# Performance work log

Hardware: AMD Instinct MI355X
Metric: run time of the kernel (lower is better)

Reference implementation:

```python
import jax, jax.numpy as jnp
import numpy as np

B, T, D, H = 8, 1024, 1024, 16
DH = D // H
EPS = 1e-5


def setup_inputs() -> dict:
    key = jax.random.key(0)
    ks = jax.random.split(key, 8)
    s = 0.02
    return {
        "x": jax.random.normal(ks[0], (B, T, D), dtype=jnp.float32),
        # per-head Q/K/V weights stacked: (H, in_c, d_head), applied as x @ W
        "Wq": jax.random.normal(ks[1], (H, D, DH), dtype=jnp.float32) * s,
        "Wk": jax.random.normal(ks[2], (H, D, DH), dtype=jnp.float32) * s,
        "Wv": jax.random.normal(ks[3], (H, D, DH), dtype=jnp.float32) * s,
        # FFN weights stored (in, out): y = x @ W
        "W1": jax.random.normal(ks[4], (D, D), dtype=jnp.float32) * s,
        "W2": jax.random.normal(ks[5], (D, D), dtype=jnp.float32) * s,
        "g1": jnp.ones((D,), jnp.float32),
        "b1": jnp.zeros((D,), jnp.float32),
        "g2": jnp.ones((D,), jnp.float32),
        "b2": jnp.zeros((D,), jnp.float32),
    }


def _layer_norm(x, g, b):
    m = jnp.mean(x, axis=-1, keepdims=True)
    v = jnp.mean((x - m) ** 2, axis=-1, keepdims=True)  # biased, as torch LN
    return (x - m) * jax.lax.rsqrt(v + EPS) * g + b


def reference(x, Wq, Wk, Wv, W1, W2, g1, b1, g2, b2):
    b, t, d = x.shape
    dh = Wq.shape[-1]
    q = jnp.einsum("btc,hcd->bhtd", x, Wq)
    k = jnp.einsum("btc,hcd->bhtd", x, Wk)
    v = jnp.einsum("btc,hcd->bhtd", x, Wv)
    attn = jnp.einsum("bhtd,bhsd->bhts", q, k) / (dh ** 0.5)
    # Original: attn @ ones(T,T) -> every column equals rowsum(attn);
    # softmax(dim=1) over the query axis is then constant across columns,
    # so out[t] = softmax_t(rowsum)[t] * sum_s v[s]. Same math, reduced.
    rowsum = attn.sum(axis=-1)               # (B,H,T)
    p = jax.nn.softmax(rowsum, axis=-1)      # softmax over query index t
    vsum = v.sum(axis=2)                     # (B,H,DH)
    head_out = p[..., None] * vsum[:, :, None, :]        # (B,H,T,DH)
    out = head_out.transpose(0, 2, 1, 3).reshape(b, t, d)  # concat heads
    x1 = _layer_norm(x + out, g1, b1)
    ff = jax.nn.relu(x1 @ W1) @ W2           # dropout = identity (eval)
    return _layer_norm(x1 + ff, g2, b2)
```

## Files before the change

### kernel.cpp

```cpp
#include <hip/hip_runtime.h>

#define NB 8
#define NT 1024
#define ND 1024
#define NH 16
#define NDH 64
#define NM (NB*NT)
#define LNEPS 1e-5f

typedef __attribute__((ext_vector_type(8))) __bf16 bf16x8;
typedef __attribute__((ext_vector_type(4))) float f32x4;

__global__ void transpose_to_bf16(const float* __restrict__ W1, const float* __restrict__ W2,
                                  __bf16* __restrict__ WT1, __bf16* __restrict__ WT2) {
    __shared__ float tile[32][33];
    const float* W = blockIdx.z ? W2 : W1;
    __bf16* WT = blockIdx.z ? WT2 : WT1;
    int bx = blockIdx.x * 32;
    int by = blockIdx.y * 32;
    int tx = threadIdx.x;
    int ty = threadIdx.y;
    for (int i = ty; i < 32; i += 8)
        tile[i][tx] = W[(size_t)(by + i) * ND + bx + tx];
    __syncthreads();
    for (int i = ty; i < 32; i += 8)
        WT[(size_t)(bx + i) * ND + by + tx] = (__bf16)tile[tx][i];
}

__global__ void xsum_kernel(const float* __restrict__ x, float* __restrict__ xsum) {
    int b = blockIdx.x;
    int chunk = blockIdx.y;
    int tid = threadIdx.x;
    const float4* xp = (const float4*)(x + ((size_t)b * NT + chunk * 16) * ND) + tid;
    float4 s = {0.f, 0.f, 0.f, 0.f};
    #pragma unroll
    for (int t = 0; t < 16; ++t) {
        float4 v = xp[(size_t)t * (ND / 4)];
        s.x += v.x; s.y += v.y; s.z += v.z; s.w += v.w;
    }
    float* dst = xsum + b * ND + tid * 4;
    atomicAdd(dst + 0, s.x);
    atomicAdd(dst + 1, s.y);
    atomicAdd(dst + 2, s.z);
    atomicAdd(dst + 3, s.w);
}

__global__ __launch_bounds__(256) void ksum_vsum_kernel(const float* __restrict__ xsum,
                                                        const float* __restrict__ Wk,
                                                        const float* __restrict__ Wv,
                                                        float* __restrict__ ksumg,
                                                        float* __restrict__ vsumg) {
    int h = blockIdx.x, cs = blockIdx.y;
    int t = threadIdx.x, lane = t & 63, w = t >> 6;
    int c0 = cs * 64;
    __shared__ float xs[8][64];
    #pragma unroll
    for (int i = 0; i < 2; ++i) {
        int idx = t + i * 256;
        xs[idx >> 6][idx & 63] = xsum[(idx >> 6) * ND + c0 + (idx & 63)];
    }
    __syncthreads();
    float sk[8] = {}, sv[8] = {};
    #pragma unroll 4
    for (int j = 0; j < 16; ++j) {
        int c = c0 + w * 16 + j;
        float wk = Wk[((size_t)h * ND + c) * NDH + lane];
        float wv = Wv[((size_t)h * ND + c) * NDH + lane];
        #pragma unroll
        for (int b = 0; b < 8; ++b) {
            float xv = xs[b][w * 16 + j];
            sk[b] += xv * wk;
            sv[b] += xv * wv;
        }
    }
    __shared__ float red[2][8][4][64];
    #pragma unroll
    for (int b = 0; b < 8; ++b) {
        red[0][b][w][lane] = sk[b];
        red[1][b][w][lane] = sv[b];
    }
    __syncthreads();
    #pragma unroll
    for (int i = 0; i < 4; ++i) {
        int o = t + i * 256;
        int d = o & 63, rest = o >> 6;
        int a = rest >> 3, b = rest & 7;
        float s = red[a][b][0][d] + red[a][b][1][d] + red[a][b][2][d] + red[a][b][3][d];
        float* dst = a ? vsumg : ksumg;
        atomicAdd(&dst[((size_t)b * NH + h) * NDH + d], s);
    }
}

__global__ __launch_bounds__(256) void wqk_kernel(const float* __restrict__ ksumg,
                                                  const float* __restrict__ Wq,
                                                  float* __restrict__ wqk) {
    int h = blockIdx.x, b = blockIdx.y, cs = blockIdx.z;
    int t = threadIdx.x;
    __shared__ float ks[NDH];
    if (t < 64) ks[t] = ksumg[((size_t)b * NH + h) * NDH + t];
    __syncthreads();
    #pragma unroll
    for (int i = 0; i < 2; ++i) {
        int c = cs * 512 + i * 256 + t;
        const float4* wq = (const float4*)(Wq + ((size_t)h * ND + c) * NDH);
        float s = 0.f;
        #pragma unroll
        for (int dq = 0; dq < 16; ++dq) {
            float4 v = wq[dq];
            s += v.x * ks[dq * 4] + v.y * ks[dq * 4 + 1] +
                 v.z * ks[dq * 4 + 2] + v.w * ks[dq * 4 + 3];
        }
        wqk[((size_t)b * NH + h) * ND + c] = s * 0.125f;
    }
}

__global__ __launch_bounds__(256) void rowsum_kernel(const float* __restrict__ x,
                                                     const float* __restrict__ wqk,
                                                     float* __restrict__ rowsum) {
    int tc = blockIdx.x, b = blockIdx.y;
    int tid = threadIdx.x, wid = tid >> 6, lane = tid & 63;
    int t0 = tc * 16 + wid * 4;
    float acc[4][16];
    #pragma unroll
    for (int tq = 0; tq < 4; ++tq)
        #pragma unroll
        for (int h = 0; h < 16; ++h) acc[tq][h] = 0.f;
    const float4* wb = (const float4*)(wqk + (size_t)b * NH * ND);
    #pragma unroll
    for (int chunk = 0; chunk < 4; ++chunk) {
        float4 xv[4];
        #pragma unroll
        for (int tq = 0; tq < 4; ++tq)
            xv[tq] = ((const float4*)(x + ((size_t)b * NT + t0 + tq) * ND))[chunk * 64 + lane];
        #pragma unroll
        for (int h = 0; h < 16; ++h) {
            float4 wv = wb[h * 256 + chunk * 64 + lane];
            #pragma unroll
            for (int tq = 0; tq < 4; ++tq)
                acc[tq][h] += xv[tq].x * wv.x + xv[tq].y * wv.y +
                              xv[tq].z * wv.z + xv[tq].w * wv.w;
        }
    }
    bool c0 = lane & 1, c1 = lane & 2, c2 = lane & 4, c3 = lane & 8;
    float out4[4];
    #pragma unroll
    for (int tq = 0; tq < 4; ++tq) {
        float w8[8];
        #pragma unroll
        for (int j = 0; j < 8; ++j) {
            float send = c0 ? acc[tq][2 * j] : acc[tq][2 * j + 1];
            float recv = __shfl_xor(send, 1, 64);
            w8[j] = (c0 ? acc[tq][2 * j + 1] : acc[tq][2 * j]) + recv;
        }
        float u4[4];
        #pragma unroll
        for (int j = 0; j < 4; ++j) {
            float send = c1 ? w8[2 * j] : w8[2 * j + 1];
            float recv = __shfl_xor(send, 2, 64);
            u4[j] = (c1 ? w8[2 * j + 1] : w8[2 * j]) + recv;
        }
        float s2[2];
        #pragma unroll
        for (int j = 0; j < 2; ++j) {
            float send = c2 ? u4[2 * j] : u4[2 * j + 1];
            float recv = __shfl_xor(send, 4, 64);
            s2[j] = (c2 ? u4[2 * j + 1] : u4[2 * j]) + recv;
        }
        float send = c3 ? s2[0] : s2[1];
        float recv = __shfl_xor(send, 8, 64);
        float r = (c3 ? s2[1] : s2[0]) + recv;
        r += __shfl_xor(r, 16, 64);
        r += __shfl_xor(r, 32, 64);
        out4[tq] = r;
    }
    if (lane < 16) {
        float4 o = {out4[0], out4[1], out4[2], out4[3]};
        *(float4*)(rowsum + ((size_t)b * NH + lane) * NT + t0) = o;
    }
}

__global__ void softmax_kernel(float* __restrict__ rs) {
    int bh = blockIdx.x, tid = threadIdx.x;
    int wave = tid >> 6, lane = tid & 63;
    float* row = rs + (size_t)bh * NT;
    float4 v = ((float4*)row)[tid];
    float m = fmaxf(fmaxf(v.x, v.y), fmaxf(v.z, v.w));
    __shared__ float red[4];
    for (int off = 32; off; off >>= 1) m = fmaxf(m, __shfl_down(m, off, 64));
    if (lane == 0) red[wave] = m;
    __syncthreads();
    m = fmaxf(fmaxf(red[0], red[1]), fmaxf(red[2], red[3]));
    __syncthreads();
    float4 e;
    e.x = __expf(v.x - m); e.y = __expf(v.y - m);
    e.z = __expf(v.z - m); e.w = __expf(v.w - m);
    float s = e.x + e.y + e.z + e.w;
    for (int off = 32; off; off >>= 1) s += __shfl_down(s, off, 64);
    if (lane == 0) red[wave] = s;
    __syncthreads();
    s = red[0] + red[1] + red[2] + red[3];
    float inv = 1.f / s;
    e.x *= inv; e.y *= inv; e.z *= inv; e.w *= inv;
    ((float4*)row)[tid] = e;
}

__global__ void ln1_kernel(const float* __restrict__ x, const float* __restrict__ p,
                           const float* __restrict__ vsum,
                           const float* __restrict__ g1, const float* __restrict__ b1,
                           __bf16* __restrict__ x1b) {
    int t = blockIdx.x, b = blockIdx.y, tid = threadIdx.x;
    int wave = tid >> 6, lane = tid & 63;
    size_t rowoff = ((size_t)b * NT + t) * ND;
    float4 xv = ((const float4*)(x + rowoff))[tid];
    int h = tid >> 4;
    float pv = p[((size_t)b * NH + h) * NT + t];
    float4 vs = ((const float4*)(vsum + ((size_t)b * NH + h) * NDH))[tid & 15];
    float4 s;
    s.x = xv.x + pv * vs.x; s.y = xv.y + pv * vs.y;
    s.z = xv.z + pv * vs.z; s.w = xv.w + pv * vs.w;
    float sum = s.x + s.y + s.z + s.w;
    float sq = s.x * s.x + s.y * s.y + s.z * s.z + s.w * s.w;
    __shared__ float rs_[4], rq_[4];
    for (int off = 32; off; off >>= 1) {
        sum += __shfl_down(sum, off, 64);
        sq += __shfl_down(sq, off, 64);
    }
    if (lane == 0) { rs_[wave] = sum; rq_[wave] = sq; }
    __syncthreads();
    sum = rs_[0] + rs_[1] + rs_[2] + rs_[3];
    sq = rq_[0] + rq_[1] + rq_[2] + rq_[3];
    float mu = sum * (1.f / ND);
    float var = sq * (1.f / ND) - mu * mu;
    float rstd = rsqrtf(var + LNEPS);
    float4 g = ((const float4*)g1)[tid];
    float4 bb = ((const float4*)b1)[tid];
    union { __bf16 h4[4]; uint2 u; } pk;
    pk.h4[0] = (__bf16)((s.x - mu) * rstd * g.x + bb.x);
    pk.h4[1] = (__bf16)((s.y - mu) * rstd * g.y + bb.y);
    pk.h4[2] = (__bf16)((s.z - mu) * rstd * g.z + bb.z);
    pk.h4[3] = (__bf16)((s.w - mu) * rstd * g.w + bb.w);
    ((uint2*)(x1b + rowoff))[tid] = pk.u;
}

template <int RELU>
__global__ __launch_bounds__(256) void gemm_bf16(const __bf16* __restrict__ A,
                                                 const __bf16* __restrict__ BT,
                                                 __bf16* __restrict__ Cout) {
    const int K = 1024, N = 1024;
    __shared__ __bf16 As[128 * 64];
    __shared__ __bf16 Bs[128 * 64];
    int raw = blockIdx.x;
    int swz = (raw & 7) * 64 + (raw >> 3);
    int m0 = (swz >> 3) * 128;
    int n0 = (swz & 7) * 128;
    int tid = threadIdx.x;
    int wid = tid >> 6, lane = tid & 63;
    int wr = wid >> 1, wc = wid & 1;
    int r = lane & 15, g = lane >> 4;
    int srow = tid >> 3;
    int soff_e = (((tid & 7) * 16) ^ ((srow & 7) << 4)) >> 1;
    const __bf16* Ag = A + (size_t)(m0 + srow) * K + soff_e;
    const __bf16* Bg = BT + (size_t)(n0 + srow) * K + soff_e;
    int swz_r = (r & 7) << 4;
    f32x4 acc[4][4] = {};
    for (int k0 = 0; k0 < K; k0 += 64) {
        __syncthreads();
        #pragma unroll
        for (int j = 0; j < 4; ++j) {
            __builtin_amdgcn_global_load_lds(
                (const __attribute__((address_space(1))) unsigned int*)(Ag + (size_t)(j * 32) * K + k0),
                (__attribute__((address_space(3))) unsigned int*)&As[(j * 32 + wid * 8) * 64], 16, 0, 0);
            __builtin_amdgcn_global_load_lds(
                (const __attribute__((address_space(1))) unsigned int*)(Bg + (size_t)(j * 32) * K + k0),
                (__attribute__((address_space(3))) unsigned int*)&Bs[(j * 32 + wid * 8) * 64], 16, 0, 0);
        }
        __syncthreads();
        #pragma unroll
        for (int ks = 0; ks < 2; ++ks) {
            int ob = (ks * 64 + g * 16) ^ swz_r;
            bf16x8 af[4], bf[4];
            #pragma unroll
            for (int mf = 0; mf < 4; ++mf)
                af[mf] = *(const bf16x8*)((const char*)&As[(wr * 64 + mf * 16 + r) * 64] + ob);
            #pragma unroll
            for (int nf = 0; nf < 4; ++nf)
                bf[nf] = *(const bf16x8*)((const char*)&Bs[(wc * 64 + nf * 16 + r) * 64] + ob);
            #pragma unroll
            for (int mf = 0; mf < 4; ++mf)
                #pragma unroll
                for (int nf = 0; nf < 4; ++nf)
                    acc[mf][nf] = __builtin_amdgcn_mfma_f32_16x16x32_bf16(af[mf], bf[nf], acc[mf][nf], 0, 0, 0);
        }
    }
    #pragma unroll
    for (int mf = 0; mf < 4; ++mf) {
        #pragma unroll
        for (int nf = 0; nf < 4; ++nf) {
            int col = n0 + wc * 64 + nf * 16 + r;
            #pragma unroll
            for (int i = 0; i < 4; ++i) {
                int row = m0 + wr * 64 + mf * 16 + g * 4 + i;
                float v = acc[mf][nf][i];
                if (RELU) v = fmaxf(v, 0.f);
                Cout[(size_t)row * N + col] = (__bf16)v;
            }
        }
    }
}

__global__ void ln2_kernel(const __bf16* __restrict__ x1b, const __bf16* __restrict__ ffb,
                           float* __restrict__ out,
                           const float* __restrict__ g2, const float* __restrict__ b2) {
    int t = blockIdx.x, b = blockIdx.y, tid = threadIdx.x;
    int wave = tid >> 6, lane = tid & 63;
    size_t rowoff = ((size_t)b * NT + t) * ND;
    union { __bf16 h4[4]; uint2 u; } pk, pf;
    pk.u = ((const uint2*)(x1b + rowoff))[tid];
    pf.u = ((const uint2*)(ffb + rowoff))[tid];
    float4 s;
    s.x = (float)pk.h4[0] + (float)pf.h4[0];
    s.y = (float)pk.h4[1] + (float)pf.h4[1];
    s.z = (float)pk.h4[2] + (float)pf.h4[2];
    s.w = (float)pk.h4[3] + (float)pf.h4[3];
    float sum = s.x + s.y + s.z + s.w;
    float sq = s.x * s.x + s.y * s.y + s.z * s.z + s.w * s.w;
    __shared__ float rs_[4], rq_[4];
    for (int off = 32; off; off >>= 1) {
        sum += __shfl_down(sum, off, 64);
        sq += __shfl_down(sq, off, 64);
    }
    if (lane == 0) { rs_[wave] = sum; rq_[wave] = sq; }
    __syncthreads();
    sum = rs_[0] + rs_[1] + rs_[2] + rs_[3];
    sq = rq_[0] + rq_[1] + rq_[2] + rq_[3];
    float mu = sum * (1.f / ND);
    float var = sq * (1.f / ND) - mu * mu;
    float rstd = rsqrtf(var + LNEPS);
    float4 g = ((const float4*)g2)[tid];
    float4 bb = ((const float4*)b2)[tid];
    float4 o;
    o.x = (s.x - mu) * rstd * g.x + bb.x;
    o.y = (s.y - mu) * rstd * g.y + bb.y;
    o.z = (s.z - mu) * rstd * g.z + bb.z;
    o.w = (s.w - mu) * rstd * g.w + bb.w;
    ((float4*)(out + rowoff))[tid] = o;
}

extern "C" void kernel_launch(void* const* d_in, const int* in_sizes, int n_in,
                              void* d_out, int out_size, void* d_ws, size_t ws_size,
                              hipStream_t stream) {
    const float* x  = (const float*)d_in[0];
    const float* Wq = (const float*)d_in[1];
    const float* Wk = (const float*)d_in[2];
    const float* Wv = (const float*)d_in[3];
    const float* W1 = (const float*)d_in[4];
    const float* W2 = (const float*)d_in[5];
    const float* g1 = (const float*)d_in[6];
    const float* b1 = (const float*)d_in[7];
    const float* g2 = (const float*)d_in[8];
    const float* b2 = (const float*)d_in[9];
    float* out = (float*)d_out;

    char* w = (char*)d_ws;
    float* xsum  = (float*)w;  w += (size_t)NB * ND * 4;
    float* ksumg = (float*)w;  w += (size_t)NB * NH * NDH * 4;
    float* vsum  = (float*)w;  w += (size_t)NB * NH * NDH * 4;
    float* wqk   = (float*)w;  w += (size_t)NB * NH * ND * 4;
    float* rsum  = (float*)w;  w += (size_t)NB * NH * NT * 4;
    __bf16* x1b = (__bf16*)w;  w += (size_t)NM * ND * 2;
    __bf16* h1b = (__bf16*)w;  w += (size_t)NM * ND * 2;
    __bf16* ffb = (__bf16*)w;  w += (size_t)NM * ND * 2;
    __bf16* w1t = (__bf16*)w;  w += (size_t)ND * ND * 2;
    __bf16* w2t = (__bf16*)w;  w += (size_t)ND * ND * 2;

    hipMemsetAsync(xsum, 0, (size_t)(NB * ND + 2 * NB * NH * NDH) * 4, stream);

    transpose_to_bf16<<<dim3(32, 32, 2), dim3(32, 8), 0, stream>>>(W1, W2, w1t, w2t);

    xsum_kernel<<<dim3(NB, 64), 256, 0, stream>>>(x, xsum);
    ksum_vsum_kernel<<<dim3(NH, 16), 256, 0, stream>>>(xsum, Wk, Wv, ksumg, vsum);
    wqk_kernel<<<dim3(NH, NB, 2), 256, 0, stream>>>(ksumg, Wq, wqk);
    rowsum_kernel<<<dim3(64, NB), 256, 0, stream>>>(x, wqk, rsum);
    softmax_kernel<<<NB * NH, 256, 0, stream>>>(rsum);
    ln1_kernel<<<dim3(NT, NB), 256, 0, stream>>>(x, rsum, vsum, g1, b1, x1b);

    gemm_bf16<1><<<512, 256, 0, stream>>>(x1b, w1t, h1b);
    gemm_bf16<0><<<512, 256, 0, stream>>>(h1b, w2t, ffb);
    ln2_kernel<<<dim3(NT, NB), 256, 0, stream>>>(x1b, ffb, out, g2, b2);
}
```

Measured before the change: 223.8 us.

## Triple-buffer GEMM with async LDS prefetch and larger 128x256 tiles

The FFN GEMM now uses 128x256 output tiles with 512 threads (8 waves) and a three-stage LDS ring buffer. Global-to-LDS loads are issued two tiles ahead, and waits use explicit vmcnt counts plus a single barrier per k-step, replacing the load-then-sync loop. s_setprio is raised around the MFMA block. The aim is to hide global memory latency and cut barrier stalls, at the cost of high LDS use (about 144KB) that limits the kernel to one block per CU, and only 256 blocks for the device.

```diff
diff --git a/kernel.cpp b/kernel.cpp
--- a/kernel.cpp
+++ b/kernel.cpp
@@ -243,55 +243,84 @@
 }
 
 template <int RELU>
-__global__ __launch_bounds__(256) void gemm_bf16(const __bf16* __restrict__ A,
-                                                 const __bf16* __restrict__ BT,
-                                                 __bf16* __restrict__ Cout) {
+__global__ __launch_bounds__(512, 1) void gemm_bf16(const __bf16* __restrict__ A,
+                                                    const __bf16* __restrict__ BT,
+                                                    __bf16* __restrict__ Cout) {
     const int K = 1024, N = 1024;
-    __shared__ __bf16 As[128 * 64];
-    __shared__ __bf16 Bs[128 * 64];
+    const int NTILES = K / 64;
+    const int BUFE = (128 + 256) * 64;
+    __shared__ __bf16 lds[3 * BUFE];
     int raw = blockIdx.x;
-    int swz = (raw & 7) * 64 + (raw >> 3);
-    int m0 = (swz >> 3) * 128;
-    int n0 = (swz & 7) * 128;
+    int swz = (raw & 7) * 32 + (raw >> 3);
+    int m0 = (swz >> 2) * 128;
+    int n0 = (swz & 3) * 256;
     int tid = threadIdx.x;
     int wid = tid >> 6, lane = tid & 63;
-    int wr = wid >> 1, wc = wid & 1;
+    int wr = wid >> 2, wc = wid & 3;
     int r = lane & 15, g = lane >> 4;
     int srow = tid >> 3;
     int soff_e = (((tid & 7) * 16) ^ ((srow & 7) << 4)) >> 1;
     const __bf16* Ag = A + (size_t)(m0 + srow) * K + soff_e;
     const __bf16* Bg = BT + (size_t)(n0 + srow) * K + soff_e;
+    int ldst = wid * 512;
     int swz_r = (r & 7) << 4;
     f32x4 acc[4][4] = {};
-    for (int k0 = 0; k0 < K; k0 += 64) {
-        __syncthreads();
-        #pragma unroll
-        for (int j = 0; j < 4; ++j) {
-            __builtin_amdgcn_global_load_lds(
-                (const __attribute__((address_space(1))) unsigned int*)(Ag + (size_t)(j * 32) * K + k0),
-                (__attribute__((address_space(3))) unsigned int*)&As[(j * 32 + wid * 8) * 64], 16, 0, 0);
-            __builtin_amdgcn_global_load_lds(
-                (const __attribute__((address_space(1))) unsigned int*)(Bg + (size_t)(j * 32) * K + k0),
-                (__attribute__((address_space(3))) unsigned int*)&Bs[(j * 32 + wid * 8) * 64], 16, 0, 0);
-        }
-        __syncthreads();
+
+    #define GL(gp, le)                                                              \
+        __builtin_amdgcn_global_load_lds(                                           \
+            (const __attribute__((address_space(1))) unsigned int*)(gp),            \
+            (__attribute__((address_space(3))) unsigned int*)&lds[le], 16, 0, 0)
+    #define STAGE(tile, buf) do {                                                   \
+        const __bf16* ag_ = Ag + (size_t)(tile) * 64;                               \
+        const __bf16* bg_ = Bg + (size_t)(tile) * 64;                               \
+        int ab_ = (buf) * BUFE, bb_ = ab_ + 128 * 64;                               \
+        GL(ag_,                 ab_ + ldst);                                        \
+        GL(ag_ + (size_t)64*K,  ab_ + 4096 + ldst);                                 \
+        GL(bg_,                 bb_ + ldst);                                        \
+        GL(bg_ + (size_t)64*K,  bb_ + 4096 + ldst);                                 \
+        GL(bg_ + (size_t)128*K, bb_ + 8192 + ldst);                                 \
+        GL(bg_ + (size_t)192*K, bb_ + 12288 + ldst);                                \
+    } while (0)
+
+    STAGE(0, 0);
+    STAGE(1, 1);
+    int cur = 0;
+    for (int t = 0; t < NTILES; ++t) {
+        if (t < NTILES - 1) {
+            asm volatile("s_waitcnt vmcnt(6)" ::: "memory");
+        } else {
+            asm volatile("s_waitcnt vmcnt(0)" ::: "memory");
+        }
+        __builtin_amdgcn_s_barrier();
+        if (t + 2 < NTILES) {
+            int nb = cur + 2; if (nb >= 3) nb -= 3;
+            STAGE(t + 2, nb);
+        }
+        const __bf16* la = &lds[cur * BUFE];
+        const __bf16* lb = la + 128 * 64;
         #pragma unroll
         for (int ks = 0; ks < 2; ++ks) {
             int ob = (ks * 64 + g * 16) ^ swz_r;
             bf16x8 af[4], bf[4];
             #pragma unroll
             for (int mf = 0; mf < 4; ++mf)
-                af[mf] = *(const bf16x8*)((const char*)&As[(wr * 64 + mf * 16 + r) * 64] + ob);
+                af[mf] = *(const bf16x8*)((const char*)&la[(wr * 64 + mf * 16 + r) * 64] + ob);
             #pragma unroll
             for (int nf = 0; nf < 4; ++nf)
-                bf[nf] = *(const bf16x8*)((const char*)&Bs[(wc * 64 + nf * 16 + r) * 64] + ob);
+                bf[nf] = *(const bf16x8*)((const char*)&lb[(wc * 64 + nf * 16 + r) * 64] + ob);
+            __builtin_amdgcn_s_setprio(1);
             #pragma unroll
             for (int mf = 0; mf < 4; ++mf)
                 #pragma unroll
                 for (int nf = 0; nf < 4; ++nf)
                     acc[mf][nf] = __builtin_amdgcn_mfma_f32_16x16x32_bf16(af[mf], bf[nf], acc[mf][nf], 0, 0, 0);
-        }
-    }
+            __builtin_amdgcn_s_setprio(0);
+        }
+        ++cur; if (cur >= 3) cur = 0;
+    }
+    #undef STAGE
+    #undef GL
+
     #pragma unroll
     for (int mf = 0; mf < 4; ++mf) {
         #pragma unroll
@@ -384,7 +413,7 @@
     softmax_kernel<<<NB * NH, 256, 0, stream>>>(rsum);
     ln1_kernel<<<dim3(NT, NB), 256, 0, stream>>>(x, rsum, vsum, g1, b1, x1b);
 
-    gemm_bf16<1><<<512, 256, 0, stream>>>(x1b, w1t, h1b);
-    gemm_bf16<0><<<512, 256, 0, stream>>>(h1b, w2t, ffb);
+    gemm_bf16<1><<<256, 512, 0, stream>>>(x1b, w1t, h1b);
+    gemm_bf16<0><<<256, 512, 0, stream>>>(h1b, w2t, ffb);
     ln2_kernel<<<dim3(NT, NB), 256, 0, stream>>>(x1b, ffb, out, g2, b2);
 }
```

After: 219.9 us. About the same (-1.8%).
